# Performance work log

Hardware: AMD Instinct MI355X
Metric: run time of the kernel (lower is better)

## Reference

```python
import jax, jax.numpy as jnp
import numpy as np

EPS = 1e-08


def setup_inputs() -> dict:
    key = jax.random.key(0)
    x = jax.random.normal(key, (16384, 1024), dtype=jnp.float32)
    return {"x": x}


def reference(x) -> jnp.ndarray:
    # L2-normalize rows (torch F.normalize clamps the norm by eps=1e-12)
    norm = jnp.maximum(jnp.linalg.norm(x, axis=-1, keepdims=True), 1e-12)
    xn = x / norm
    # B x B cosine similarity
    sim = xn @ xn.T
    # exclude self-similarity on the diagonal
    B = sim.shape[0]
    diag = jnp.eye(B, dtype=bool)
    sim = jnp.where(diag, -jnp.inf, sim)
    max_sim = jnp.max(sim, axis=1)
    # squared L2 distance to nearest neighbor on the unit sphere
    distances = jnp.sqrt(2.0 - 2.0 * max_sim + EPS)
    return -jnp.mean(jnp.log(distances))
```

## Files before the change

### kernel.cpp

```cpp
#include <hip/hip_runtime.h>
#include <hip/hip_bf16.h>

#define NROWS 16384
#define DIM   1024
#define NT    8
#define NTILE 128
#define NBLK  (NTILE * (NTILE + 1) / 2)
#define SW    16

typedef int i32x4 __attribute__((ext_vector_type(4)));

__device__ __forceinline__ unsigned fkey(float f) {
    unsigned u = __float_as_uint(f);
    return (u & 0x80000000u) ? ~u : (u | 0x80000000u);
}
__device__ __forceinline__ float funkey(unsigned k) {
    unsigned u = (k & 0x80000000u) ? (k & 0x7fffffffu) : ~k;
    return __uint_as_float(u);
}

__global__ void normalize_rows(const float* __restrict__ x,
                               signed char* __restrict__ xq,
                               float* __restrict__ sinv,
                               unsigned* __restrict__ rowmax) {
    const int row = blockIdx.x;
    const int t = threadIdx.x;
    const float4 v = ((const float4*)(x + (size_t)row * DIM))[t];
    float ss = v.x * v.x + v.y * v.y + v.z * v.z + v.w * v.w;
#pragma unroll
    for (int off = 32; off > 0; off >>= 1) ss += __shfl_xor(ss, off);
    __shared__ float wss[4];
    __shared__ int   wqs[4];
    if ((t & 63) == 0) wss[t >> 6] = ss;
    __syncthreads();
    const float tot = wss[0] + wss[1] + wss[2] + wss[3];
    const float scale = 127.0f / fmaxf(sqrtf(tot), 1e-12f);
    int qx = __float2int_rn(v.x * scale);
    int qy = __float2int_rn(v.y * scale);
    int qz = __float2int_rn(v.z * scale);
    int qw = __float2int_rn(v.w * scale);
    qx = max(-127, min(127, qx)); qy = max(-127, min(127, qy));
    qz = max(-127, min(127, qz)); qw = max(-127, min(127, qw));
    const int p = (qx & 0xff) | ((qy & 0xff) << 8) | ((qz & 0xff) << 16) | ((qw & 0xff) << 24);
    ((int*)(xq + (size_t)row * DIM))[t] = p;
    int qs = qx * qx + qy * qy + qz * qz + qw * qw;
#pragma unroll
    for (int off = 32; off > 0; off >>= 1) qs += __shfl_xor(qs, off);
    if ((t & 63) == 0) wqs[t >> 6] = qs;
    __syncthreads();
    if (t == 0) {
        const int qtot = max(wqs[0] + wqs[1] + wqs[2] + wqs[3], 1);
        sinv[row] = 1.0f / sqrtf((float)qtot);
        rowmax[row] = 0u;
    }
}


__global__ __launch_bounds__(256, 4)
void simmax_kernel(const signed char* __restrict__ xq,
                   const float* __restrict__ sinv,
                   unsigned* __restrict__ rowmax) {
    const int bid = blockIdx.x;
    int rem = (bid & 7) * (NBLK / 8) + (bid >> 3);
    int s = 0;
    for (;;) {
        const int sz = 256 * s + 136;
        if (rem < sz) break;
        rem -= sz;
        ++s;
    }
    int it, jt;
    const int full = 256 * s;
    if (rem < full) {
        it = rem >> 4;
        jt = SW * s + (rem & 15);
    } else {
        int r2 = rem - full;
        int d = 0;
        while (r2 >= SW - d) { r2 -= SW - d; ++d; }
        it = SW * s + d;
        jt = it + r2;
    }
    const bool diag = (jt == it);
    const int rowBase = it * 128;
    const int colBase = jt * 128;

    __shared__ __align__(16) char lds[2][128][128];

    const int t    = threadIdx.x;
    const int lane = t & 63;
    const int wid  = t >> 6;
    const int wr2  = wid >> 1;
    const int wc2  = wid & 1;
    const int l15  = lane & 15;
    const int hi   = lane >> 4;

    const signed char* srcp[8];
#pragma unroll
    for (int j = 0; j < 8; ++j) {
        const int c   = j * 256 + t;
        const int op  = c >> 10;
        const int cc  = c & 1023;
        const int row = cc >> 3;
        const int ch  = cc & 7;
        const int gr  = (op ? colBase : rowBase) + row;
        srcp[j] = xq + (size_t)gr * DIM + (ch ^ (row & 7)) * 16;
    }

    i32x4 acc[4][4];
#pragma unroll
    for (int m = 0; m < 4; ++m)
#pragma unroll
        for (int n = 0; n < 4; ++n)
            acc[m][n] = (i32x4){0, 0, 0, 0};

    char* ldsb = &lds[0][0][0];

    for (int kt = 0; kt < NT; ++kt) {
        __syncthreads();
#pragma unroll
        for (int j = 0; j < 8; ++j) {
            __builtin_amdgcn_global_load_lds(
                (const __attribute__((address_space(1))) void*)srcp[j],
                (__attribute__((address_space(3))) void*)(ldsb + (j * 256 + wid * 64) * 16),
                16, 0, 0);
            srcp[j] += 128;
        }
        __syncthreads();

        i32x4 af[4][2], bf[4][2];
#pragma unroll
        for (int m = 0; m < 4; ++m)
#pragma unroll
            for (int kk = 0; kk < 2; ++kk) {
                const int row = wr2 * 64 + m * 16 + l15;
                const int chn = (kk * 4 + hi) ^ (row & 7);
                af[m][kk] = *(const i32x4*)(&lds[0][0][0] + row * 128 + chn * 16);
            }
#pragma unroll
        for (int n = 0; n < 4; ++n)
#pragma unroll
            for (int kk = 0; kk < 2; ++kk) {
                const int row = wc2 * 64 + n * 16 + l15;
                const int chn = (kk * 4 + hi) ^ (row & 7);
                bf[n][kk] = *(const i32x4*)(&lds[1][0][0] + row * 128 + chn * 16);
            }
#pragma unroll
        for (int m = 0; m < 4; ++m)
#pragma unroll
            for (int n = 0; n < 4; ++n)
#pragma unroll
                for (int kk = 0; kk < 2; ++kk)
                    acc[m][n] = __builtin_amdgcn_mfma_i32_16x16x64_i8(
                        af[m][kk], bf[n][kk], acc[m][n], 0, 0, 0);
    }

    const int g  = lane >> 4;
    const int cl = lane & 15;

    float scl_col[4];
#pragma unroll
    for (int n = 0; n < 4; ++n)
        scl_col[n] = sinv[colBase + wc2 * 64 + n * 16 + cl];
    float srow[4][4];
#pragma unroll
    for (int m = 0; m < 4; ++m)
#pragma unroll
        for (int r = 0; r < 4; ++r)
            srow[m][r] = sinv[rowBase + wr2 * 64 + m * 16 + g * 4 + r];

#pragma unroll
    for (int m = 0; m < 4; ++m)
#pragma unroll
        for (int r = 0; r < 4; ++r) {
            const int grow = wr2 * 64 + m * 16 + g * 4 + r;
            float v = -1e30f;
#pragma unroll
            for (int n = 0; n < 4; ++n) {
                const int gcol = wc2 * 64 + n * 16 + cl;
                float f = (float)acc[m][n][r] * scl_col[n];
                if (diag && grow == gcol) f = -1e30f;
                v = fmaxf(v, f);
            }
            v = fmaxf(v, __shfl_xor(v, 1));
            v = fmaxf(v, __shfl_xor(v, 2));
            v = fmaxf(v, __shfl_xor(v, 4));
            v = fmaxf(v, __shfl_xor(v, 8));
            if (cl == 0) atomicMax(rowmax + rowBase + grow, fkey(v));
        }

    if (!diag) {
#pragma unroll
        for (int n = 0; n < 4; ++n) {
            float v = -1e30f;
#pragma unroll
            for (int m = 0; m < 4; ++m)
#pragma unroll
                for (int r = 0; r < 4; ++r)
                    v = fmaxf(v, (float)acc[m][n][r] * srow[m][r]);
            v = fmaxf(v, __shfl_xor(v, 16));
            v = fmaxf(v, __shfl_xor(v, 32));
            if (g == 0) {
                const int gcol = colBase + wc2 * 64 + n * 16 + cl;
                atomicMax(rowmax + gcol, fkey(v));
            }
        }
    }
}

__global__ void finalize_kernel(const unsigned* __restrict__ rowmax,
                                const float* __restrict__ sinv,
                                float* __restrict__ out) {
    const int t = threadIdx.x;
    float s = 0.f;
    for (int r = t; r < NROWS; r += 256) {
        const float m = fminf(sinv[r] * funkey(rowmax[r]), 1.0f);
        s += logf(2.0f - 2.0f * m + 1e-8f);
    }
#pragma unroll
    for (int off = 32; off > 0; off >>= 1) s += __shfl_xor(s, off);
    __shared__ float ws[4];
    if ((t & 63) == 0) ws[t >> 6] = s;
    __syncthreads();
    if (t == 0) out[0] = -0.5f * (ws[0] + ws[1] + ws[2] + ws[3]) / (float)NROWS;
}

extern "C" void kernel_launch(void* const* d_in, const int* in_sizes, int n_in,
                              void* d_out, int out_size, void* d_ws, size_t ws_size,
                              hipStream_t stream) {
    const float* x = (const float*)d_in[0];
    signed char* xq = (signed char*)d_ws;
    float* sinv = (float*)((char*)d_ws + (size_t)NROWS * DIM);
    unsigned* rowmax = (unsigned*)((char*)d_ws + (size_t)NROWS * DIM + NROWS * sizeof(float));
    float* out = (float*)d_out;

    normalize_rows<<<NROWS, 256, 0, stream>>>(x, xq, sinv, rowmax);
    simmax_kernel<<<NBLK, 256, 0, stream>>>(xq, sinv, rowmax);
    finalize_kernel<<<1, 256, 0, stream>>>(rowmax, sinv, out);
}
```

Before: 246.5 us.

## Double-buffer LDS tiles with prefetch and reduce row maxima in shared memory

Switches the int8 GEMM K-loop to double-buffered LDS: the next K-slice is issued with global_load_lds while MFMAs run on the current one, so each iteration needs one barrier instead of two. It also raises wave priority around the MFMA block and lowers the launch-bounds occupancy hint from 4 to 2. The epilogue now combines row and column maxima in a shared-memory array before issuing one global atomicMax per row or column, cutting global atomic traffic. LDS use doubles, which may reduce the number of resident blocks per CU.

```diff
diff --git a/kernel.cpp b/kernel.cpp
--- a/kernel.cpp
+++ b/kernel.cpp
@@ -56,7 +56,9 @@
 }
 
 
-__global__ __launch_bounds__(256, 4)
+#define SB() __builtin_amdgcn_sched_barrier(0)
+
+__global__ __launch_bounds__(256, 2)
 void simmax_kernel(const signed char* __restrict__ xq,
                    const float* __restrict__ sinv,
                    unsigned* __restrict__ rowmax) {
@@ -85,7 +87,8 @@
     const int rowBase = it * 128;
     const int colBase = jt * 128;
 
-    __shared__ __align__(16) char lds[2][128][128];
+    __shared__ __align__(16) char lds[2][2][128][128];
+    __shared__ unsigned redmax[256];
 
     const int t    = threadIdx.x;
     const int lane = t & 63;
@@ -94,6 +97,8 @@
     const int wc2  = wid & 1;
     const int l15  = lane & 15;
     const int hi   = lane >> 4;
+
+    redmax[t] = 0u;
 
     const signed char* srcp[8];
 #pragma unroll
@@ -107,6 +112,18 @@
         srcp[j] = xq + (size_t)gr * DIM + (ch ^ (row & 7)) * 16;
     }
 
+#pragma unroll
+    for (int j = 0; j < 8; ++j) {
+        __builtin_amdgcn_global_load_lds(
+            (const __attribute__((address_space(1))) void*)srcp[j],
+            (__attribute__((address_space(3))) void*)(&lds[0][0][0][0] + (j * 256 + wid * 64) * 16),
+            16, 0, 0);
+        srcp[j] += 128;
+    }
+    asm volatile("s_waitcnt vmcnt(0)" ::: "memory");
+    __builtin_amdgcn_s_barrier();
+    SB();
+
     i32x4 acc[4][4];
 #pragma unroll
     for (int m = 0; m < 4; ++m)
@@ -114,19 +131,10 @@
         for (int n = 0; n < 4; ++n)
             acc[m][n] = (i32x4){0, 0, 0, 0};
 
-    char* ldsb = &lds[0][0][0];
-
-    for (int kt = 0; kt < NT; ++kt) {
-        __syncthreads();
-#pragma unroll
-        for (int j = 0; j < 8; ++j) {
-            __builtin_amdgcn_global_load_lds(
-                (const __attribute__((address_space(1))) void*)srcp[j],
-                (__attribute__((address_space(3))) void*)(ldsb + (j * 256 + wid * 64) * 16),
-                16, 0, 0);
-            srcp[j] += 128;
-        }
-        __syncthreads();
+    for (int tk = 0; tk < NT; ++tk) {
+        char* curb = &lds[tk & 1][0][0][0];
+        char* nxtb = &lds[(tk & 1) ^ 1][0][0][0];
+        const bool pf = (tk + 1 < NT);
 
         i32x4 af[4][2], bf[4][2];
 #pragma unroll
@@ -135,16 +143,37 @@
             for (int kk = 0; kk < 2; ++kk) {
                 const int row = wr2 * 64 + m * 16 + l15;
                 const int chn = (kk * 4 + hi) ^ (row & 7);
-                af[m][kk] = *(const i32x4*)(&lds[0][0][0] + row * 128 + chn * 16);
-            }
+                af[m][kk] = *(const i32x4*)(curb + row * 128 + chn * 16);
+            }
+        if (pf) {
+#pragma unroll
+            for (int j = 0; j < 4; ++j) {
+                __builtin_amdgcn_global_load_lds(
+                    (const __attribute__((address_space(1))) void*)srcp[j],
+                    (__attribute__((address_space(3))) void*)(nxtb + (j * 256 + wid * 64) * 16),
+                    16, 0, 0);
+                srcp[j] += 128;
+            }
+        }
 #pragma unroll
         for (int n = 0; n < 4; ++n)
 #pragma unroll
             for (int kk = 0; kk < 2; ++kk) {
                 const int row = wc2 * 64 + n * 16 + l15;
                 const int chn = (kk * 4 + hi) ^ (row & 7);
-                bf[n][kk] = *(const i32x4*)(&lds[1][0][0] + row * 128 + chn * 16);
-            }
+                bf[n][kk] = *(const i32x4*)(curb + 16384 + row * 128 + chn * 16);
+            }
+        if (pf) {
+#pragma unroll
+            for (int j = 4; j < 8; ++j) {
+                __builtin_amdgcn_global_load_lds(
+                    (const __attribute__((address_space(1))) void*)srcp[j],
+                    (__attribute__((address_space(3))) void*)(nxtb + (j * 256 + wid * 64) * 16),
+                    16, 0, 0);
+                srcp[j] += 128;
+            }
+        }
+        __builtin_amdgcn_s_setprio(1);
 #pragma unroll
         for (int m = 0; m < 4; ++m)
 #pragma unroll
@@ -153,6 +182,11 @@
                 for (int kk = 0; kk < 2; ++kk)
                     acc[m][n] = __builtin_amdgcn_mfma_i32_16x16x64_i8(
                         af[m][kk], bf[n][kk], acc[m][n], 0, 0, 0);
+        __builtin_amdgcn_s_setprio(0);
+
+        asm volatile("s_waitcnt vmcnt(0)" ::: "memory");
+        __builtin_amdgcn_s_barrier();
+        SB();
     }
 
     const int g  = lane >> 4;
@@ -186,7 +220,7 @@
             v = fmaxf(v, __shfl_xor(v, 2));
             v = fmaxf(v, __shfl_xor(v, 4));
             v = fmaxf(v, __shfl_xor(v, 8));
-            if (cl == 0) atomicMax(rowmax + rowBase + grow, fkey(v));
+            if (cl == 0) atomicMax(&redmax[grow], fkey(v));
         }
 
     if (!diag) {
@@ -200,11 +234,16 @@
                     v = fmaxf(v, (float)acc[m][n][r] * srow[m][r]);
             v = fmaxf(v, __shfl_xor(v, 16));
             v = fmaxf(v, __shfl_xor(v, 32));
-            if (g == 0) {
-                const int gcol = colBase + wc2 * 64 + n * 16 + cl;
-                atomicMax(rowmax + gcol, fkey(v));
-            }
-        }
+            if (g == 0) atomicMax(&redmax[128 + wc2 * 64 + n * 16 + cl], fkey(v));
+        }
+    }
+    __syncthreads();
+
+    const unsigned k = redmax[t];
+    if (t < 128) {
+        atomicMax(rowmax + rowBase + t, k);
+    } else if (!diag) {
+        atomicMax(rowmax + colBase + (t - 128), k);
     }
 }
 
```

After: 256.8 us. 1.04x slower.
